# Optimization experiments

Hardware: AMD Instinct MI355X
Metric: run time of the kernel (lower is better)

Reference implementation:

```python
import jax, jax.numpy as jnp
import numpy as np

V, BLK, H, D, L = 32000, 1024, 16, 1024, 3
HD = D // H  # 64
B, T = 4, 1024


def _layernorm(x, g, b, eps=1e-5):
    mu = jnp.mean(x, axis=-1, keepdims=True)
    var = jnp.mean(jnp.square(x - mu), axis=-1, keepdims=True)
    return (x - mu) * jax.lax.rsqrt(var + eps) * g + b


def setup_inputs() -> dict:
    key = jax.random.key(0)
    ks = jax.random.split(key, 32)
    s = 0.02
    inp = {}
    inp["idx"] = jax.random.randint(ks[0], (B, T), 0, V)
    inp["target"] = jax.random.randint(ks[1], (B, T), 0, V)
    inp["tok_emb"] = jax.random.normal(ks[2], (V, D), jnp.float32) * s
    inp["pos_emb"] = jax.random.normal(ks[3], (BLK, D), jnp.float32) * s
    inp["wq"] = jax.random.normal(ks[4], (L, H, D, HD), jnp.float32) * s
    inp["wk"] = jax.random.normal(ks[5], (L, H, D, HD), jnp.float32) * s
    inp["wv"] = jax.random.normal(ks[6], (L, H, D, HD), jnp.float32) * s
    inp["wproj"] = jax.random.normal(ks[7], (L, D, D), jnp.float32) * s
    inp["bproj"] = jnp.zeros((L, D), jnp.float32)
    inp["ln1_g"] = jnp.ones((L, D), jnp.float32)
    inp["ln1_b"] = jnp.zeros((L, D), jnp.float32)
    inp["ln2_g"] = jnp.ones((L, D), jnp.float32)
    inp["ln2_b"] = jnp.zeros((L, D), jnp.float32)
    inp["w1"] = jax.random.normal(ks[8], (L, D, 4 * D), jnp.float32) * s
    inp["b1"] = jnp.zeros((L, 4 * D), jnp.float32)
    inp["w2"] = jax.random.normal(ks[9], (L, 4 * D, D), jnp.float32) * s
    inp["b2"] = jnp.zeros((L, D), jnp.float32)
    inp["lnf_g"] = jnp.ones((D,), jnp.float32)
    inp["lnf_b"] = jnp.zeros((D,), jnp.float32)
    inp["wlm"] = jax.random.normal(ks[10], (D, V), jnp.float32) * s
    inp["blm"] = jnp.zeros((V,), jnp.float32)
    return inp


def reference(idx, target, tok_emb, pos_emb, wq, wk, wv, wproj, bproj,
              ln1_g, ln1_b, ln2_g, ln2_b, w1, b1, w2, b2,
              lnf_g, lnf_b, wlm, blm):
    Bb, Tt = idx.shape
    x = tok_emb[idx] + pos_emb[:Tt]  # [B,T,D]
    mask = jnp.tril(jnp.ones((Tt, Tt), dtype=bool))  # causal
    scale = D ** -0.5  # NOTE: source scales by n_embd**-0.5, not head_size**-0.5
    for l in range(L):
        xn = _layernorm(x, ln1_g[l], ln1_b[l])
        q = jnp.einsum('btd,hde->bhte', xn, wq[l])
        k = jnp.einsum('btd,hde->bhte', xn, wk[l])
        v = jnp.einsum('btd,hde->bhte', xn, wv[l])
        scores = jnp.einsum('bhte,bhse->bhts', q, k) * scale
        scores = jnp.where(mask, scores, -jnp.inf)
        attn = jax.nn.softmax(scores, axis=-1)
        o = jnp.einsum('bhts,bhse->bhte', attn, v)
        o = o.transpose(0, 2, 1, 3).reshape(Bb, Tt, D)  # concat heads
        x = x + o @ wproj[l] + bproj[l]
        xn2 = _layernorm(x, ln2_g[l], ln2_b[l])
        h = jax.nn.relu(xn2 @ w1[l] + b1[l])
        x = x + h @ w2[l] + b2[l]
    x = _layernorm(x, lnf_g, lnf_b)
    logits = x @ wlm + blm  # [B,T,V]
    logp = jax.nn.log_softmax(logits, axis=-1)
    nll = -jnp.take_along_axis(logp, target[..., None], axis=-1)[..., 0]
    loss = jnp.mean(nll)
    return logits, loss
```

## Files before the change

### kernel.cpp

```cpp
#include <hip/hip_runtime.h>
#include <math.h>

#define Dn   1024
#define Hn   16
#define HDn  64
#define Tn   1024
#define Bn   4
#define Vn   32000
#define Ln   3
#define NT   (Bn*Tn)

typedef __attribute__((ext_vector_type(8))) short bf16x8;
typedef __attribute__((ext_vector_type(4))) float f32x4;

__device__ __forceinline__ float b2f(unsigned short u) {
  union { float f; unsigned int i; } c; c.i = ((unsigned int)u) << 16; return c.f;
}
__device__ __forceinline__ unsigned short f2b(float f) {
  union { float f; unsigned int i; } c; c.f = f;
  unsigned int r = (c.i + 0x7FFFu + ((c.i >> 16) & 1u)) >> 16;
  return (unsigned short)r;
}

#define GLOAD_LDS16(g, l) __builtin_amdgcn_global_load_lds( \
    (const __attribute__((address_space(1))) void*)(g),     \
    (__attribute__((address_space(3))) void*)(l), 16, 0, 0)

#define SBAR()  __builtin_amdgcn_s_barrier()
#define SCHED() __builtin_amdgcn_sched_barrier(0)

__global__ __launch_bounds__(256) void embed_kernel(
    const int* __restrict__ idx, const float* __restrict__ tok,
    const float* __restrict__ pos, float* __restrict__ x) {
  int row = blockIdx.x;
  int t = row & (Tn - 1);
  int token = idx[row];
  const float4* tp = (const float4*)(tok + (size_t)token * Dn);
  const float4* pp = (const float4*)(pos + (size_t)t * Dn);
  float4* xp = (float4*)(x + (size_t)row * Dn);
  int i = threadIdx.x;
  float4 a = tp[i], b = pp[i];
  xp[i] = make_float4(a.x + b.x, a.y + b.y, a.z + b.z, a.w + b.w);
}

__global__ __launch_bounds__(256) void ln_kernel(
    const float* __restrict__ x, const float* __restrict__ g,
    const float* __restrict__ b, unsigned short* __restrict__ y) {
  int row = blockIdx.x;
  const float4* xr = (const float4*)(x + (size_t)row * Dn);
  __shared__ float red[4];
  int lane = threadIdx.x & 63, w = threadIdx.x >> 6;

  float4 v = xr[threadIdx.x];
  float s = v.x + v.y + v.z + v.w;
  #pragma unroll
  for (int o = 32; o > 0; o >>= 1) s += __shfl_down(s, o, 64);
  if (lane == 0) red[w] = s;
  __syncthreads();
  float mu = (red[0] + red[1] + red[2] + red[3]) * (1.0f / Dn);
  __syncthreads();

  float dx = v.x - mu, dy = v.y - mu, dz = v.z - mu, dw = v.w - mu;
  float ss = dx*dx + dy*dy + dz*dz + dw*dw;
  #pragma unroll
  for (int o = 32; o > 0; o >>= 1) ss += __shfl_down(ss, o, 64);
  if (lane == 0) red[w] = ss;
  __syncthreads();
  float var = (red[0] + red[1] + red[2] + red[3]) * (1.0f / Dn);
  float inv = rsqrtf(var + 1e-5f);

  float4 gv = ((const float4*)g)[threadIdx.x];
  float4 bv = ((const float4*)b)[threadIdx.x];
  ushort4 o4;
  o4.x = f2b(dx*inv*gv.x + bv.x);
  o4.y = f2b(dy*inv*gv.y + bv.y);
  o4.z = f2b(dz*inv*gv.z + bv.z);
  o4.w = f2b(dw*inv*gv.w + bv.w);
  ((ushort4*)(y + (size_t)row * Dn))[threadIdx.x] = o4;
}

__global__ __launch_bounds__(256) void wcast_kernel(
    const float* __restrict__ src, unsigned short* __restrict__ dst,
    int K, int M, long long bsk, long long bsh) {
  __shared__ float t[32][33];
  int m0 = blockIdx.x << 5, k0 = blockIdx.y << 5;
  int tid = threadIdx.x;
  int ml = tid & 31, kl = tid >> 5;
  #pragma unroll
  for (int p = 0; p < 4; ++p) {
    int k = k0 + kl + p * 8;
    int m = m0 + ml;
    t[ml][kl + p * 8] = src[(size_t)k * bsk + (size_t)(m >> 6) * bsh + (m & 63)];
  }
  __syncthreads();
  int kl2 = tid & 31, ml2 = tid >> 5;
  #pragma unroll
  for (int p = 0; p < 4; ++p) {
    int m = m0 + ml2 + p * 8;
    int k = k0 + kl2;
    dst[(size_t)m * K + k] = f2b(t[ml2 + p * 8][kl2]);
  }
}

__global__ __launch_bounds__(256) void mm_bf16(
    const unsigned short* __restrict__ A, const unsigned short* __restrict__ BT,
    const float* __restrict__ bias, const float* __restrict__ res,
    float* __restrict__ Cf, unsigned short* __restrict__ Ch,
    int N, int K, int M, int relu) {
  __shared__ __align__(16) unsigned short As[3][128 * 32];
  __shared__ __align__(16) unsigned short Bs[3][128 * 32];
  const int tid = threadIdx.x;
  const int lane = tid & 63, w = tid >> 6, g = lane >> 4;
  const int wr = w >> 1, wc = w & 1;
  const int n0 = blockIdx.x << 7, m0 = blockIdx.y << 7;

  f32x4 acc[4][4];
  #pragma unroll
  for (int i = 0; i < 4; ++i)
    #pragma unroll
    for (int j = 0; j < 4; ++j)
      acc[i][j] = (f32x4){0.f, 0.f, 0.f, 0.f};

  const int beta0 = w * 2048 + lane * 16;
  const int beta1 = beta0 + 1024;
  const int r0 = beta0 >> 6, u0 = (beta0 >> 4) & 3;
  const int r1 = beta1 >> 6, u1 = (beta1 >> 4) & 3;
  const int ks0 = u0 ^ ((r0 >> 1) & 3);
  const int ks1 = u1 ^ ((r1 >> 1) & 3);
  const unsigned short* a_g0 = A + (size_t)(n0 + r0) * K + ks0 * 8;
  const unsigned short* a_g1 = A + (size_t)(n0 + r1) * K + ks1 * 8;
  const unsigned short* b_g0 = BT + (size_t)(m0 + r0) * K + ks0 * 8;
  const unsigned short* b_g1 = BT + (size_t)(m0 + r1) * K + ks1 * 8;

  int a_off[4], b_off[4];
  #pragma unroll
  for (int f = 0; f < 4; ++f) {
    int row = wr * 64 + f * 16 + (lane & 15);
    a_off[f] = row * 64 + ((g ^ ((row >> 1) & 3)) << 4);
    int col = wc * 64 + f * 16 + (lane & 15);
    b_off[f] = col * 64 + ((g ^ ((col >> 1) & 3)) << 4);
  }

#define MM_STAGE(buf, kk) do {                                   \
    GLOAD_LDS16(a_g0 + (kk), As[buf] + w * 1024);                \
    GLOAD_LDS16(a_g1 + (kk), As[buf] + w * 1024 + 512);          \
    GLOAD_LDS16(b_g0 + (kk), Bs[buf] + w * 1024);                \
    GLOAD_LDS16(b_g1 + (kk), Bs[buf] + w * 1024 + 512); } while (0)

#define MM_COMPUTE(buf) do {                                     \
    bf16x8 af[4], bfr[4];                                        \
    _Pragma("unroll")                                            \
    for (int f = 0; f < 4; ++f) {                                \
      af[f]  = *(const bf16x8*)((const char*)As[buf] + a_off[f]);\
      bfr[f] = *(const bf16x8*)((const char*)Bs[buf] + b_off[f]);\
    }                                                            \
    _Pragma("unroll")                                            \
    for (int i = 0; i < 4; ++i)                                  \
      _Pragma("unroll")                                          \
      for (int j = 0; j < 4; ++j)                                \
        acc[i][j] = __builtin_amdgcn_mfma_f32_16x16x32_bf16(af[i], bfr[j], acc[i][j], 0, 0, 0); } while (0)

  MM_STAGE(0, 0);
  MM_STAGE(1, 32);
  int bc = 0, bp = 2;
  for (int k0 = 0; k0 < K; k0 += 32) {
    if (k0 + 64 < K) {
      MM_STAGE(bp, k0 + 64);
      asm volatile("s_waitcnt vmcnt(8)" ::: "memory");
    } else if (k0 + 32 < K) {
      asm volatile("s_waitcnt vmcnt(4)" ::: "memory");
    } else {
      asm volatile("s_waitcnt vmcnt(0)" ::: "memory");
    }
    SCHED(); SBAR(); SCHED();
    MM_COMPUTE(bc);
    SCHED(); SBAR(); SCHED();
    bc = (bc == 2) ? 0 : bc + 1;
    bp = (bp == 2) ? 0 : bp + 1;
  }

  #pragma unroll
  for (int fc = 0; fc < 4; ++fc) {
    int colg = m0 + wc * 64 + fc * 16 + (lane & 15);
    float bz = bias ? bias[colg] : 0.f;
    #pragma unroll
    for (int fr = 0; fr < 4; ++fr) {
      #pragma unroll
      for (int i = 0; i < 4; ++i) {
        int rowg = n0 + wr * 64 + fr * 16 + (g << 2) + i;
        float v = acc[fr][fc][i] + bz;
        if (res) v += res[(size_t)rowg * M + colg];
        if (relu) v = fmaxf(v, 0.f);
        if (Cf) Cf[(size_t)rowg * M + colg] = v;
        else    Ch[(size_t)rowg * M + colg] = f2b(v);
      }
    }
  }
#undef MM_STAGE
#undef MM_COMPUTE
}

template<int OMODE>
__global__ __launch_bounds__(512) void mm512_bf16(
    const unsigned short* __restrict__ A, const unsigned short* __restrict__ BT,
    const float* __restrict__ bias, const float* __restrict__ res,
    float* __restrict__ Cf, unsigned short* __restrict__ Ch,
    float* __restrict__ rowsum, int N, int K, int M, int relu) {
  __shared__ __align__(16) unsigned short As[3][128 * 32];
  __shared__ __align__(16) unsigned short Bs[3][256 * 32];
  __shared__ float rsum2[OMODE == 4 ? 128 * 4 : 4];
  const int tid = threadIdx.x;
  const int lane = tid & 63, w = tid >> 6, g = lane >> 4;
  const int wr = w >> 2, wc = w & 3;
  const int n0 = blockIdx.x << 7, m0 = blockIdx.y << 8;

  f32x4 acc[4][4];
  #pragma unroll
  for (int i = 0; i < 4; ++i)
    #pragma unroll
    for (int j = 0; j < 4; ++j)
      acc[i][j] = (f32x4){0.f, 0.f, 0.f, 0.f};

  const int arow = tid >> 2, au = tid & 3;
  const int aks = au ^ ((arow >> 1) & 3);
  const unsigned short* a_g = A + (size_t)(n0 + arow) * K + aks * 8;
  const int brow1 = (tid + 512) >> 2;
  const int bks0 = au ^ ((arow >> 1) & 3);
  const int bks1 = au ^ ((brow1 >> 1) & 3);
  const unsigned short* b_g0 = BT + (size_t)(m0 + arow) * K + bks0 * 8;
  const unsigned short* b_g1 = BT + (size_t)(m0 + brow1) * K + bks1 * 8;

  int a_off[4], b_off[4];
  #pragma unroll
  for (int f = 0; f < 4; ++f) {
    int row = wr * 64 + f * 16 + (lane & 15);
    a_off[f] = row * 64 + ((g ^ ((row >> 1) & 3)) << 4);
    int col = wc * 64 + f * 16 + (lane & 15);
    b_off[f] = col * 64 + ((g ^ ((col >> 1) & 3)) << 4);
  }

#define MM5_STAGE(buf, kk) do {                                  \
    GLOAD_LDS16(a_g + (kk), As[buf] + tid * 8);                  \
    GLOAD_LDS16(b_g0 + (kk), Bs[buf] + tid * 8);                 \
    GLOAD_LDS16(b_g1 + (kk), Bs[buf] + (tid + 512) * 8); } while (0)

#define MM5_COMPUTE(buf) do {                                    \
    bf16x8 af[4], bfr[4];                                        \
    _Pragma("unroll")                                            \
    for (int f = 0; f < 4; ++f) {                                \
      af[f]  = *(const bf16x8*)((const char*)As[buf] + a_off[f]);\
      bfr[f] = *(const bf16x8*)((const char*)Bs[buf] + b_off[f]);\
    }                                                            \
    _Pragma("unroll")                                            \
    for (int i = 0; i < 4; ++i)                                  \
      _Pragma("unroll")                                          \
      for (int j = 0; j < 4; ++j)                                \
        acc[i][j] = __builtin_amdgcn_mfma_f32_16x16x32_bf16(af[i], bfr[j], acc[i][j], 0, 0, 0); } while (0)

  MM5_STAGE(0, 0);
  MM5_STAGE(1, 32);
  int bc = 0, bp = 2;
  for (int k0 = 0; k0 < K; k0 += 32) {
    if (k0 + 64 < K) {
      MM5_STAGE(bp, k0 + 64);
      asm volatile("s_waitcnt vmcnt(6)" ::: "memory");
    } else if (k0 + 32 < K) {
      asm volatile("s_waitcnt vmcnt(3)" ::: "memory");
    } else {
      asm volatile("s_waitcnt vmcnt(0)" ::: "memory");
    }
    SCHED(); SBAR(); SCHED();
    MM5_COMPUTE(bc);
    SCHED(); SBAR(); SCHED();
    bc = (bc == 2) ? 0 : bc + 1;
    bp = (bp == 2) ? 0 : bp + 1;
  }

  if (OMODE == 0) {
    #pragma unroll
    for (int fc = 0; fc < 4; ++fc) {
      int colg = m0 + wc * 64 + fc * 16 + (lane & 15);
      float bz = bias ? bias[colg] : 0.f;
      #pragma unroll
      for (int fr = 0; fr < 4; ++fr) {
        #pragma unroll
        for (int i = 0; i < 4; ++i) {
          int rowg = n0 + wr * 64 + fr * 16 + (g << 2) + i;
          float v = acc[fr][fc][i] + bz;
          if (res) v += res[(size_t)rowg * M + colg];
          if (relu) v = fmaxf(v, 0.f);
          if (Cf) Cf[(size_t)rowg * M + colg] = v;
          else    Ch[(size_t)rowg * M + colg] = f2b(v);
        }
      }
    }
  } else if (OMODE == 3) {
    unsigned short* kb  = Ch + (size_t)NT * Dn;
    unsigned short* vtb = Ch + 2 * (size_t)NT * Dn;
    #pragma unroll
    for (int fc = 0; fc < 4; ++fc) {
      int colg = m0 + wc * 64 + fc * 16 + (lane & 15);
      int sel = colg >> 10, hh = (colg >> 6) & 15, e = colg & 63;
      #pragma unroll
      for (int fr = 0; fr < 4; ++fr) {
        int rowg0 = n0 + wr * 64 + fr * 16 + (g << 2);
        int b = rowg0 >> 10, t0 = rowg0 & 1023;
        if (sel == 2) {
          ushort4 pk;
          pk.x = f2b(acc[fr][fc][0]); pk.y = f2b(acc[fr][fc][1]);
          pk.z = f2b(acc[fr][fc][2]); pk.w = f2b(acc[fr][fc][3]);
          *(ushort4*)&vtb[(((size_t)(b * 16 + hh) * 64) + e) * 1024 + t0] = pk;
        } else {
          unsigned short* dst = (sel == 0) ? Ch : kb;
          #pragma unroll
          for (int i = 0; i < 4; ++i)
            dst[(((size_t)(b * 16 + hh) * 1024) + t0 + i) * 64 + e] = f2b(acc[fr][fc][i]);
        }
      }
    }
  } else {
    #pragma unroll
    for (int fr = 0; fr < 4; ++fr) {
      #pragma unroll
      for (int i = 0; i < 4; ++i) {
        int rloc = wr * 64 + fr * 16 + (g << 2) + i;
        int rowg = n0 + rloc;
        float es = 0.f;
        #pragma unroll
        for (int fc = 0; fc < 4; ++fc) {
          int colg = m0 + wc * 64 + fc * 16 + (lane & 15);
          float v = acc[fr][fc][i] + bias[colg];
          __builtin_nontemporal_store(v, &Cf[(size_t)rowg * M + colg]);
          es += __expf(v);
        }
        es += __shfl_xor(es, 1); es += __shfl_xor(es, 2);
        es += __shfl_xor(es, 4); es += __shfl_xor(es, 8);
        if ((lane & 15) == 0) rsum2[rloc * 4 + wc] = es;
      }
    }
    __syncthreads();
    if (tid < 128)
      atomicAdd(&rowsum[n0 + tid],
                rsum2[tid * 4 + 0] + rsum2[tid * 4 + 1] +
                rsum2[tid * 4 + 2] + rsum2[tid * 4 + 3]);
  }
#undef MM5_STAGE
#undef MM5_COMPUTE
}

__global__ __launch_bounds__(256) void fattn_kernel(
    const unsigned short* __restrict__ qg, const unsigned short* __restrict__ kg,
    const unsigned short* __restrict__ vtg, unsigned short* __restrict__ ob) {
  const int bid = blockIdx.x;
  const int qt = bid & 15, bh = bid >> 4;
  const int b = bh >> 4, h = bh & 15;
  const int tid = threadIdx.x, lane = tid & 63, w = tid >> 6, g = lane >> 4;

  __shared__ __align__(16) unsigned short Ks[2][64 * 64];
  __shared__ __align__(16) unsigned short Vs[2][64 * 64];
  __shared__ __align__(16) unsigned short Pb[4][16 * 64];

  const unsigned short* kbase = kg + (size_t)bh * Tn * HDn;
  const unsigned short* vbase = vtg + (size_t)bh * HDn * Tn;

  const int qrow = qt * 64 + w * 16 + (lane & 15);
  const unsigned short* qptr = qg + ((size_t)bh * Tn + qrow) * HDn;
  bf16x8 qf0 = *(const bf16x8*)(qptr + g * 8);
  bf16x8 qf1 = *(const bf16x8*)(qptr + 32 + g * 8);

  f32x4 accO[4];
  #pragma unroll
  for (int dt = 0; dt < 4; ++dt) accO[dt] = (f32x4){0.f, 0.f, 0.f, 0.f};
  float mrun[4] = {-1e30f, -1e30f, -1e30f, -1e30f};
  float lrun[4] = {0.f, 0.f, 0.f, 0.f};

  const float scale = 0.03125f;
  const int qout0 = qt * 64 + w * 16 + 4 * g;

  unsigned short* pb = &Pb[w][0];
  const int nsteps = qt + 1;

#define FA_STAGE(buf, s0_) do {                                              \
    _Pragma("unroll")                                                        \
    for (int r = 0; r < 2; ++r) {                                            \
      int c = tid + 256 * r;                                                 \
      int srow = c >> 3, u = c & 7;                                          \
      GLOAD_LDS16(kbase + (size_t)((s0_) + srow) * HDn + ((u ^ (srow & 7)) * 8), Ks[buf] + c * 8); \
    }                                                                        \
    _Pragma("unroll")                                                        \
    for (int r = 0; r < 2; ++r) {                                            \
      int c = tid + 256 * r;                                                 \
      int d = c >> 3, u = c & 7;                                             \
      GLOAD_LDS16(vbase + (size_t)d * Tn + (s0_) + ((u ^ (d & 7)) * 8), Vs[buf] + c * 8); \
    } } while (0)

  FA_STAGE(0, 0);
  int cur = 0;

  for (int st = 0; st < nsteps; ++st) {
    const int s0 = st * 64;
    if (st + 1 < nsteps) {
      FA_STAGE(cur ^ 1, s0 + 64);
      asm volatile("s_waitcnt vmcnt(4)" ::: "memory");
    } else {
      asm volatile("s_waitcnt vmcnt(0)" ::: "memory");
    }
    SCHED(); SBAR(); SCHED();

    float p[4][4];
    #pragma unroll
    for (int sub = 0; sub < 4; ++sub) {
      int srow = sub * 16 + (lane & 15);
      const char* kr = (const char*)Ks[cur] + srow * 128;
      bf16x8 kf0 = *(const bf16x8*)(kr + ((g ^ (srow & 7)) * 16));
      bf16x8 kf1 = *(const bf16x8*)(kr + (((4 + g) ^ (srow & 7)) * 16));
      f32x4 s4 = (f32x4){0.f, 0.f, 0.f, 0.f};
      s4 = __builtin_amdgcn_mfma_f32_16x16x32_bf16(qf0, kf0, s4, 0, 0, 0);
      s4 = __builtin_amdgcn_mfma_f32_16x16x32_bf16(qf1, kf1, s4, 0, 0, 0);
      int sg = s0 + srow;
      #pragma unroll
      for (int i = 0; i < 4; ++i)
        p[sub][i] = (sg > qout0 + i) ? -1e30f : s4[i] * scale;
    }

    #pragma unroll
    for (int i = 0; i < 4; ++i) {
      float v = fmaxf(fmaxf(p[0][i], p[1][i]), fmaxf(p[2][i], p[3][i]));
      v = fmaxf(v, __shfl_xor(v, 1)); v = fmaxf(v, __shfl_xor(v, 2));
      v = fmaxf(v, __shfl_xor(v, 4)); v = fmaxf(v, __shfl_xor(v, 8));
      float nm = fmaxf(mrun[i], v);
      float fac = __expf(mrun[i] - nm);
      mrun[i] = nm;
      #pragma unroll
      for (int dt = 0; dt < 4; ++dt) accO[dt][i] *= fac;
      float sum = 0.f;
      #pragma unroll
      for (int sub = 0; sub < 4; ++sub) {
        float e = __expf(p[sub][i] - nm);
        p[sub][i] = e;
        sum += e;
      }
      sum += __shfl_xor(sum, 1); sum += __shfl_xor(sum, 2);
      sum += __shfl_xor(sum, 4); sum += __shfl_xor(sum, 8);
      lrun[i] = lrun[i] * fac + sum;
    }

    #pragma unroll
    for (int sub = 0; sub < 4; ++sub) {
      int s = sub * 16 + (lane & 15);
      #pragma unroll
      for (int i = 0; i < 4; ++i) {
        int q = 4 * g + i;
        pb[q * 64 + (((s >> 3) ^ (q & 7)) * 8) + (s & 7)] = f2b(p[sub][i]);
      }
    }

    #pragma unroll
    for (int sc = 0; sc < 2; ++sc) {
      int qq = lane & 15;
      bf16x8 pa = *(const bf16x8*)((const char*)pb + qq * 128 + (((sc * 4 + g) ^ (qq & 7)) * 16));
      #pragma unroll
      for (int dt = 0; dt < 4; ++dt) {
        int d = dt * 16 + (lane & 15);
        bf16x8 vf = *(const bf16x8*)((const char*)Vs[cur] + d * 128 + (((sc * 4 + g) ^ (d & 7)) * 16));
        accO[dt] = __builtin_amdgcn_mfma_f32_16x16x32_bf16(pa, vf, accO[dt], 0, 0, 0);
      }
    }

    SCHED(); SBAR(); SCHED();
    cur ^= 1;
  }
#undef FA_STAGE

  float rinv[4];
  #pragma unroll
  for (int i = 0; i < 4; ++i) rinv[i] = 1.0f / lrun[i];
  #pragma unroll
  for (int dt = 0; dt < 4; ++dt) {
    int dcol = h * 64 + dt * 16 + (lane & 15);
    #pragma unroll
    for (int i = 0; i < 4; ++i) {
      int t = qout0 + i;
      ob[((size_t)(b * Tn + t)) * Dn + dcol] = f2b(accO[dt][i] * rinv[i]);
    }
  }
}

__global__ __launch_bounds__(256) void loss_kernel(
    const float* __restrict__ logits, const float* __restrict__ rowsum,
    const int* __restrict__ target, float* __restrict__ out_loss) {
  __shared__ float red[4];
  int lane = threadIdx.x & 63, w = threadIdx.x >> 6;
  float s = 0.f;
  for (int row = threadIdx.x; row < NT; row += 256) {
    float lt = logits[(size_t)row * Vn + target[row]];
    s += logf(rowsum[row]) - lt;
  }
  #pragma unroll
  for (int off = 32; off > 0; off >>= 1) s += __shfl_down(s, off, 64);
  if (lane == 0) red[w] = s;
  __syncthreads();
  if (threadIdx.x == 0)
    *out_loss = (red[0] + red[1] + red[2] + red[3]) * (1.0f / NT);
}

static inline void launch_wcast(const float* src, unsigned short* dst, int K, int M,
                                long long bsk, long long bsh, hipStream_t s) {
  dim3 g(M >> 5, K >> 5);
  wcast_kernel<<<g, 256, 0, s>>>(src, dst, K, M, bsk, bsh);
}

static inline void launch_mm(const unsigned short* A, const unsigned short* BT,
                             const float* bias, const float* res,
                             float* Cf, unsigned short* Ch,
                             int N, int K, int M, int relu, hipStream_t s) {
  dim3 g(N >> 7, M >> 7);
  mm_bf16<<<g, 256, 0, s>>>(A, BT, bias, res, Cf, Ch, N, K, M, relu);
}

template<int OMODE>
static inline void launch_mm512(const unsigned short* A, const unsigned short* BT,
                                const float* bias, const float* res,
                                float* Cf, unsigned short* Ch, float* rowsum,
                                int N, int K, int M, int relu, hipStream_t s) {
  dim3 g(N >> 7, M >> 8);
  mm512_bf16<OMODE><<<g, 512, 0, s>>>(A, BT, bias, res, Cf, Ch, rowsum, N, K, M, relu);
}

extern "C" void kernel_launch(void* const* d_in, const int* in_sizes, int n_in,
                              void* d_out, int out_size, void* d_ws, size_t ws_size,
                              hipStream_t stream) {
  const int*   idx    = (const int*)d_in[0];
  const int*   target = (const int*)d_in[1];
  const float* tok    = (const float*)d_in[2];
  const float* pos    = (const float*)d_in[3];
  const float* wq     = (const float*)d_in[4];
  const float* wk     = (const float*)d_in[5];
  const float* wv     = (const float*)d_in[6];
  const float* wproj  = (const float*)d_in[7];
  const float* bproj  = (const float*)d_in[8];
  const float* ln1g   = (const float*)d_in[9];
  const float* ln1b   = (const float*)d_in[10];
  const float* ln2g   = (const float*)d_in[11];
  const float* ln2b   = (const float*)d_in[12];
  const float* w1     = (const float*)d_in[13];
  const float* b1     = (const float*)d_in[14];
  const float* w2     = (const float*)d_in[15];
  const float* b2     = (const float*)d_in[16];
  const float* lnfg   = (const float*)d_in[17];
  const float* lnfb   = (const float*)d_in[18];
  const float* wlm    = (const float*)d_in[19];
  const float* blm    = (const float*)d_in[20];

  float* out = (float*)d_out;

  char* p = (char*)d_ws;
  float* x  = (float*)p;                 p += (size_t)NT * Dn * 4;
  unsigned short* xn = (unsigned short*)p; p += (size_t)NT * Dn * 2;
  unsigned short* reg = (unsigned short*)p; p += (size_t)NT * 4 * Dn * 2;
  unsigned short* wT = (unsigned short*)p; p += (size_t)Vn * Dn * 2;
  float* rowsum = (float*)p;

  unsigned short* qb  = reg;
  unsigned short* kb  = reg + (size_t)NT * Dn;
  unsigned short* vtb = reg + 2 * (size_t)NT * Dn;
  unsigned short* ob  = reg + 3 * (size_t)NT * Dn;
  unsigned short* hb  = reg;

  embed_kernel<<<NT, 256, 0, stream>>>(idx, tok, pos, x);

  for (int l = 0; l < Ln; ++l) {
    const float* wq_l = wq + (size_t)l * Hn * Dn * HDn;
    const float* wk_l = wk + (size_t)l * Hn * Dn * HDn;
    const float* wv_l = wv + (size_t)l * Hn * Dn * HDn;

    ln_kernel<<<NT, 256, 0, stream>>>(x, ln1g + l * Dn, ln1b + l * Dn, xn);

    launch_wcast(wq_l, wT,                  Dn, Dn, HDn, (long long)Dn * HDn, stream);
    launch_wcast(wk_l, wT + 1024 * Dn,      Dn, Dn, HDn, (long long)Dn * HDn, stream);
    launch_wcast(wv_l, wT + 2048 * Dn,      Dn, Dn, HDn, (long long)Dn * HDn, stream);
    launch_mm512<3>(xn, wT, nullptr, nullptr, nullptr, qb, nullptr, NT, Dn, 3072, 0, stream);

    fattn_kernel<<<Bn * Hn * (Tn / 64), 256, 0, stream>>>(qb, kb, vtb, ob);

    launch_wcast(wproj + (size_t)l * Dn * Dn, wT, Dn, Dn, Dn, 64, stream);
    launch_mm(ob, wT, bproj + l * Dn, x, x, nullptr, NT, Dn, Dn, 0, stream);

    ln_kernel<<<NT, 256, 0, stream>>>(x, ln2g + l * Dn, ln2b + l * Dn, xn);

    launch_wcast(w1 + (size_t)l * Dn * 4 * Dn, wT, Dn, 4 * Dn, 4 * Dn, 64, stream);
    launch_mm512<0>(xn, wT, b1 + l * 4 * Dn, nullptr, nullptr, hb, nullptr, NT, Dn, 4 * Dn, 1, stream);
    launch_wcast(w2 + (size_t)l * 4 * Dn * Dn, wT, 4 * Dn, Dn, Dn, 64, stream);
    launch_mm(hb, wT, b2 + l * Dn, x, x, nullptr, NT, 4 * Dn, Dn, 0, stream);
  }

  ln_kernel<<<NT, 256, 0, stream>>>(x, lnfg, lnfb, xn);

  hipMemsetAsync(rowsum, 0, NT * sizeof(float), stream);
  launch_wcast(wlm, wT, Dn, Vn, Vn, 64, stream);
  launch_mm512<4>(xn, wT, blm, nullptr, out, nullptr, rowsum, NT, Dn, Vn, 0, stream);

  loss_kernel<<<1, 256, 0, stream>>>(out, rowsum, target, out + (size_t)NT * Vn);
}
```

Baseline: 1.291 ms.

## Widen mm_bf16 to 512 threads, single-barrier prefetch loop, fuse QKV weight casts

The 128x128 GEMM kernel now runs 8 waves of 512 threads, each owning a 64x32 sub-tile, with one 16-byte global-to-LDS load per thread per operand. In both GEMM kernels the main loop drops the second barrier and issues the next stage prefetch after the barrier, relying on triple buffering to keep it safe. The three Q/K/V weight cast-transpose launches are merged into one launch over a z-dimension of three. The aim is more latency hiding, less barrier overhead and fewer launches, at the cost of halved per-wave MFMA reuse and fragile vmcnt accounting.

Result: faster. 1.207 ms (-6.5%).

```diff
diff --git a/kernel.cpp b/kernel.cpp
--- a/kernel.cpp
+++ b/kernel.cpp
@@ -102,7 +102,32 @@
   }
 }
 
-__global__ __launch_bounds__(256) void mm_bf16(
+__global__ __launch_bounds__(256) void wcast3_kernel(
+    const float* __restrict__ s0, const float* __restrict__ s1,
+    const float* __restrict__ s2, unsigned short* __restrict__ dst) {
+  const float* src = (blockIdx.z == 0) ? s0 : (blockIdx.z == 1) ? s1 : s2;
+  unsigned short* d = dst + (size_t)blockIdx.z * 1024 * Dn;
+  __shared__ float t[32][33];
+  int m0 = blockIdx.x << 5, k0 = blockIdx.y << 5;
+  int tid = threadIdx.x;
+  int ml = tid & 31, kl = tid >> 5;
+  #pragma unroll
+  for (int p = 0; p < 4; ++p) {
+    int k = k0 + kl + p * 8;
+    int m = m0 + ml;
+    t[ml][kl + p * 8] = src[(size_t)k * HDn + (size_t)(m >> 6) * (Dn * HDn) + (m & 63)];
+  }
+  __syncthreads();
+  int kl2 = tid & 31, ml2 = tid >> 5;
+  #pragma unroll
+  for (int p = 0; p < 4; ++p) {
+    int m = m0 + ml2 + p * 8;
+    int k = k0 + kl2;
+    d[(size_t)m * Dn + k] = f2b(t[ml2 + p * 8][kl2]);
+  }
+}
+
+__global__ __launch_bounds__(512) void mm_bf16(
     const unsigned short* __restrict__ A, const unsigned short* __restrict__ BT,
     const float* __restrict__ bias, const float* __restrict__ res,
     float* __restrict__ Cf, unsigned short* __restrict__ Ch,
@@ -111,77 +136,67 @@
   __shared__ __align__(16) unsigned short Bs[3][128 * 32];
   const int tid = threadIdx.x;
   const int lane = tid & 63, w = tid >> 6, g = lane >> 4;
-  const int wr = w >> 1, wc = w & 1;
+  const int wr = w >> 2, wc = w & 3;
   const int n0 = blockIdx.x << 7, m0 = blockIdx.y << 7;
 
-  f32x4 acc[4][4];
+  f32x4 acc[4][2];
   #pragma unroll
   for (int i = 0; i < 4; ++i)
     #pragma unroll
-    for (int j = 0; j < 4; ++j)
+    for (int j = 0; j < 2; ++j)
       acc[i][j] = (f32x4){0.f, 0.f, 0.f, 0.f};
 
-  const int beta0 = w * 2048 + lane * 16;
-  const int beta1 = beta0 + 1024;
-  const int r0 = beta0 >> 6, u0 = (beta0 >> 4) & 3;
-  const int r1 = beta1 >> 6, u1 = (beta1 >> 4) & 3;
-  const int ks0 = u0 ^ ((r0 >> 1) & 3);
-  const int ks1 = u1 ^ ((r1 >> 1) & 3);
-  const unsigned short* a_g0 = A + (size_t)(n0 + r0) * K + ks0 * 8;
-  const unsigned short* a_g1 = A + (size_t)(n0 + r1) * K + ks1 * 8;
-  const unsigned short* b_g0 = BT + (size_t)(m0 + r0) * K + ks0 * 8;
-  const unsigned short* b_g1 = BT + (size_t)(m0 + r1) * K + ks1 * 8;
-
-  int a_off[4], b_off[4];
+  const int srow = tid >> 2, su = tid & 3;
+  const int sks = su ^ ((srow >> 1) & 3);
+  const unsigned short* a_g = A + (size_t)(n0 + srow) * K + sks * 8;
+  const unsigned short* b_g = BT + (size_t)(m0 + srow) * K + sks * 8;
+
+  int a_off[4], b_off[2];
   #pragma unroll
   for (int f = 0; f < 4; ++f) {
     int row = wr * 64 + f * 16 + (lane & 15);
     a_off[f] = row * 64 + ((g ^ ((row >> 1) & 3)) << 4);
-    int col = wc * 64 + f * 16 + (lane & 15);
+  }
+  #pragma unroll
+  for (int f = 0; f < 2; ++f) {
+    int col = wc * 32 + f * 16 + (lane & 15);
     b_off[f] = col * 64 + ((g ^ ((col >> 1) & 3)) << 4);
   }
 
 #define MM_STAGE(buf, kk) do {                                   \
-    GLOAD_LDS16(a_g0 + (kk), As[buf] + w * 1024);                \
-    GLOAD_LDS16(a_g1 + (kk), As[buf] + w * 1024 + 512);          \
-    GLOAD_LDS16(b_g0 + (kk), Bs[buf] + w * 1024);                \
-    GLOAD_LDS16(b_g1 + (kk), Bs[buf] + w * 1024 + 512); } while (0)
+    GLOAD_LDS16(a_g + (kk), As[buf] + tid * 8);                  \
+    GLOAD_LDS16(b_g + (kk), Bs[buf] + tid * 8); } while (0)
 
 #define MM_COMPUTE(buf) do {                                     \
-    bf16x8 af[4], bfr[4];                                        \
+    bf16x8 af[4], bfr[2];                                        \
     _Pragma("unroll")                                            \
-    for (int f = 0; f < 4; ++f) {                                \
-      af[f]  = *(const bf16x8*)((const char*)As[buf] + a_off[f]);\
+    for (int f = 0; f < 4; ++f)                                  \
+      af[f] = *(const bf16x8*)((const char*)As[buf] + a_off[f]); \
+    _Pragma("unroll")                                            \
+    for (int f = 0; f < 2; ++f)                                  \
       bfr[f] = *(const bf16x8*)((const char*)Bs[buf] + b_off[f]);\
-    }                                                            \
     _Pragma("unroll")                                            \
     for (int i = 0; i < 4; ++i)                                  \
       _Pragma("unroll")                                          \
-      for (int j = 0; j < 4; ++j)                                \
+      for (int j = 0; j < 2; ++j)                                \
         acc[i][j] = __builtin_amdgcn_mfma_f32_16x16x32_bf16(af[i], bfr[j], acc[i][j], 0, 0, 0); } while (0)
 
   MM_STAGE(0, 0);
   MM_STAGE(1, 32);
   int bc = 0, bp = 2;
   for (int k0 = 0; k0 < K; k0 += 32) {
-    if (k0 + 64 < K) {
-      MM_STAGE(bp, k0 + 64);
-      asm volatile("s_waitcnt vmcnt(8)" ::: "memory");
-    } else if (k0 + 32 < K) {
-      asm volatile("s_waitcnt vmcnt(4)" ::: "memory");
-    } else {
-      asm volatile("s_waitcnt vmcnt(0)" ::: "memory");
-    }
+    if (k0 + 32 < K) asm volatile("s_waitcnt vmcnt(2)" ::: "memory");
+    else             asm volatile("s_waitcnt vmcnt(0)" ::: "memory");
     SCHED(); SBAR(); SCHED();
+    if (k0 + 64 < K) MM_STAGE(bp, k0 + 64);
     MM_COMPUTE(bc);
-    SCHED(); SBAR(); SCHED();
     bc = (bc == 2) ? 0 : bc + 1;
     bp = (bp == 2) ? 0 : bp + 1;
   }
 
   #pragma unroll
-  for (int fc = 0; fc < 4; ++fc) {
-    int colg = m0 + wc * 64 + fc * 16 + (lane & 15);
+  for (int fc = 0; fc < 2; ++fc) {
+    int colg = m0 + wc * 32 + fc * 16 + (lane & 15);
     float bz = bias ? bias[colg] : 0.f;
     #pragma unroll
     for (int fr = 0; fr < 4; ++fr) {
@@ -261,17 +276,11 @@
   MM5_STAGE(1, 32);
   int bc = 0, bp = 2;
   for (int k0 = 0; k0 < K; k0 += 32) {
-    if (k0 + 64 < K) {
-      MM5_STAGE(bp, k0 + 64);
-      asm volatile("s_waitcnt vmcnt(6)" ::: "memory");
-    } else if (k0 + 32 < K) {
-      asm volatile("s_waitcnt vmcnt(3)" ::: "memory");
-    } else {
-      asm volatile("s_waitcnt vmcnt(0)" ::: "memory");
-    }
+    if (k0 + 32 < K) asm volatile("s_waitcnt vmcnt(3)" ::: "memory");
+    else             asm volatile("s_waitcnt vmcnt(0)" ::: "memory");
     SCHED(); SBAR(); SCHED();
+    if (k0 + 64 < K) MM5_STAGE(bp, k0 + 64);
     MM5_COMPUTE(bc);
-    SCHED(); SBAR(); SCHED();
     bc = (bc == 2) ? 0 : bc + 1;
     bp = (bp == 2) ? 0 : bp + 1;
   }
@@ -515,7 +524,7 @@
                              float* Cf, unsigned short* Ch,
                              int N, int K, int M, int relu, hipStream_t s) {
   dim3 g(N >> 7, M >> 7);
-  mm_bf16<<<g, 256, 0, s>>>(A, BT, bias, res, Cf, Ch, N, K, M, relu);
+  mm_bf16<<<g, 512, 0, s>>>(A, BT, bias, res, Cf, Ch, N, K, M, relu);
 }
 
 template<int OMODE>
@@ -576,9 +585,10 @@
 
     ln_kernel<<<NT, 256, 0, stream>>>(x, ln1g + l * Dn, ln1b + l * Dn, xn);
 
-    launch_wcast(wq_l, wT,                  Dn, Dn, HDn, (long long)Dn * HDn, stream);
-    launch_wcast(wk_l, wT + 1024 * Dn,      Dn, Dn, HDn, (long long)Dn * HDn, stream);
-    launch_wcast(wv_l, wT + 2048 * Dn,      Dn, Dn, HDn, (long long)Dn * HDn, stream);
+    {
+      dim3 g3(32, 32, 3);
+      wcast3_kernel<<<g3, 256, 0, stream>>>(wq_l, wk_l, wv_l, wT);
+    }
     launch_mm512<3>(xn, wT, nullptr, nullptr, nullptr, qb, nullptr, NT, Dn, 3072, 0, stream);
 
     fattn_kernel<<<Bn * Hn * (Tn / 64), 256, 0, stream>>>(qb, kb, vtb, ob);
```
